# Kernel tuning notes

Measured on AMD Instinct MI355X. Metric: run time of the kernel, lower is better.

Reference implementation:

```python
import jax, jax.numpy as jnp
import numpy as np

B, C_IN, H, W_SP = 16, 128, 56, 56
C_OUT, KH, KW = 256, 3, 3
STRIDE = (1, 1)
PADDING = (1, 1)


def setup_inputs() -> dict:
    key = jax.random.key(0)
    kx, kw = jax.random.split(key)
    x = jax.random.normal(kx, (B, C_IN, H, W_SP), dtype=jnp.float32)
    W = jax.random.normal(kw, (C_OUT, C_IN, KH, KW), dtype=jnp.float32) * 0.01
    b = jnp.zeros((C_OUT,), dtype=jnp.float32)
    return {"x": x, "W": W, "b": b}


def reference(x, W, b):
    # NCHW direct convolution, same math as the nested-loop torch module.
    out = jax.lax.conv_general_dilated(
        x, W,
        window_strides=STRIDE,
        padding=[(PADDING[0], PADDING[0]), (PADDING[1], PADDING[1])],
        dimension_numbers=("NCHW", "OIHW", "NCHW"),
    )
    return out + b[None, :, None, None]
```

## Files before the change

kernel.cpp:

```cpp
#include <hip/hip_runtime.h>

typedef __attribute__((ext_vector_type(8))) short short8;
typedef __attribute__((ext_vector_type(4))) float f32x4;

#define CI    128
#define CO_   256
#define HW_   56
#define PLANE 3136
#define NB    16
#define STOT  50176
#define KTOT  1152
#define OUTN  802816

#define XT_BYTES   12845056ull
#define WP_USHORTS 294912
#define WS_NEED    (12845056ull + 589824ull + 256ull)

__device__ __forceinline__ unsigned short f2bf(float f) {
  unsigned u = __float_as_uint(f);
  u += 0x7FFFu + ((u >> 16) & 1u);
  return (unsigned short)(u >> 16);
}

__device__ __forceinline__ void gload16(void* lds, const void* g) {
  __builtin_amdgcn_global_load_lds(
      (const __attribute__((address_space(1))) unsigned int*)g,
      (__attribute__((address_space(3))) unsigned int*)lds, 16, 0, 0);
}

template <int N> __device__ __forceinline__ void vmwait() {
  asm volatile("s_waitcnt vmcnt(%0)" ::"n"(N) : "memory");
}

__global__ __launch_bounds__(256) void prep_fused(const float* __restrict__ X,
                                                  const float* __restrict__ W,
                                                  unsigned short* __restrict__ Xt,
                                                  unsigned short* __restrict__ Wp) {
  const int t = threadIdx.x;
  if (blockIdx.x < 1600) {
    __shared__ __align__(16) unsigned short tile[32][132];
    const int bx = blockIdx.x;
    const int n   = bx / 100;
    const int rem = bx % 100;
    const int cib = rem / 25;
    const int spb = rem % 25;
    const int sp0 = spb * 128;
    const float* src = X + (size_t)(n * CI + cib * 32) * PLANE;
#pragma unroll
    for (int j = 0; j < 4; ++j) {
      int f = t + 256 * j;
      int ci  = f >> 5;
      int sp4 = (f & 31) * 4;
      if (sp0 + sp4 < PLANE) {
        f32x4 v = *(const f32x4*)(src + (size_t)ci * PLANE + sp0 + sp4);
#pragma unroll
        for (int e = 0; e < 4; ++e) tile[ci][sp4 + e] = f2bf(v[e]);
      }
    }
    __syncthreads();
    unsigned short* dst = Xt + ((size_t)n * PLANE + sp0) * CI + cib * 32;
#pragma unroll
    for (int j = 0; j < 2; ++j) {
      int g = t + 256 * j;
      int sp = g >> 2;
      int q  = g & 3;
      if (sp0 + sp < PLANE) {
        short8 v;
#pragma unroll
        for (int e = 0; e < 8; ++e) v[e] = (short)tile[q * 8 + e][sp];
        *(short8*)(dst + (size_t)sp * CI + q * 8) = v;
      }
    }
  } else {
    const int u = (blockIdx.x - 1600) * 256 + t;
    const int rcbmt = u >> 9;
    const int p     = u & 511;
    const int mt  = rcbmt & 1;
    const int rcb = rcbmt >> 1;
    const int cb  = rcb & 3;
    const int r   = rcb >> 2;
    const int col = p >> 2;
    const int kg  = (p & 3) ^ ((col >> 1) & 3);
    const int co  = mt * 128 + col;
    const int ci0 = cb * 32 + kg * 8;
    short8 v;
#pragma unroll
    for (int e = 0; e < 8; ++e)
      v[e] = (short)f2bf(W[(size_t)co * KTOT + (size_t)(ci0 + e) * 9 + r]);
    *(short8*)(Wp + (size_t)u * 8) = v;
    if (u < 16) {
      short8 z = {0, 0, 0, 0, 0, 0, 0, 0};
      *(short8*)(Wp + WP_USHORTS + u * 8) = z;
    }
  }
}

__global__ __launch_bounds__(512, 2) void conv_gemm(const unsigned short* __restrict__ Xt,
                                                    const unsigned short* __restrict__ Wp,
                                                    const float* __restrict__ bias,
                                                    float* __restrict__ out) {
  __shared__ __align__(1024) char smem[131072];
  const int t    = threadIdx.x;
  const int lane = t & 63;
  const int wid  = t >> 6;
  const int wm   = wid >> 2, wn = wid & 3;

  const int orig = blockIdx.x;
  const int xcd = orig & 7, idx = orig >> 3;
  const int spt = (xcd < 4 ? xcd * 25 : 100 + (xcd - 4) * 24) + idx;

  const int kgB = (t & 3) ^ ((t >> 3) & 3);
  const int S0 = spt * 256 + (t >> 2);
  const int S1 = S0 + 128;
  const int hw0 = S0 % PLANE, h0 = hw0 / HW_, w0 = hw0 - h0 * HW_;
  const int hw1 = S1 % PLANE, h1 = hw1 / HW_, w1 = hw1 - h1 * HW_;
  int vm0 = 0, vm1 = 0;
#pragma unroll
  for (int r = 0; r < 9; ++r) {
    int dh = r / 3 - 1, dw = r % 3 - 1;
    vm0 |= (int)(((unsigned)(h0 + dh) < HW_) & ((unsigned)(w0 + dw) < HW_)) << r;
    vm1 |= (int)(((unsigned)(h1 + dh) < HW_) & ((unsigned)(w1 + dw) < HW_)) << r;
  }
  const char* xb0 = (const char*)Xt + ((size_t)S0 * CI + kgB * 8) * 2;
  const char* xb1 = (const char*)Xt + ((size_t)S1 * CI + kgB * 8) * 2;
  const char* zb  = (const char*)(Wp + WP_USHORTS) + (t & 3) * 16;
  const char* wpA = (const char*)Wp + t * 16;

  const int swz  = ((lane >> 4) ^ ((lane >> 1) & 3)) * 16;
  const int aoff = (wm * 128 + (lane & 15)) * 64 + swz;
  const int boff = 16384 + (wn * 64 + (lane & 15)) * 64 + swz;

  f32x4 acc[8][4];
  const f32x4 zf = {0.f, 0.f, 0.f, 0.f};
#pragma unroll
  for (int m = 0; m < 8; ++m)
#pragma unroll
    for (int n = 0; n < 4; ++n) acc[m][n] = zf;

  auto SA = [&](int s1, int j, char* buf) {
    gload16(buf + j * 8192 + wid * 1024, wpA + (size_t)s1 * 16384 + j * 8192);
  };
  auto SB = [&](int s1, int j, char* buf) {
    const int r = s1 >> 2, cb = s1 & 3;
    const int dh = r / 3 - 1, dw = r % 3 - 1;
    const int ro = dh * HW_ + dw;
    const bool v = ((j ? vm1 : vm0) >> r) & 1;
    const char* src = (j ? xb1 : xb0) + ro * 256 + cb * 64;
    gload16(buf + 16384 + j * 8192 + wid * 1024, v ? src : zb);
  };
  auto STAGE = [&](int s1) {
    char* nb = smem + (s1 & 3) * 32768;
    SA(s1, 0, nb); SA(s1, 1, nb); SB(s1, 0, nb); SB(s1, 1, nb);
  };

  STAGE(0); STAGE(1); STAGE(2);

#pragma unroll
  for (int s = 0; s < 36; ++s) {
    if (s <= 34) vmwait<4>();
    else         vmwait<0>();
    __builtin_amdgcn_s_barrier();

    if (s <= 32) STAGE(s + 3);

    const char* rb = smem + (s & 3) * 32768;
    short8 bF[4];
#pragma unroll
    for (int n = 0; n < 4; ++n) bF[n] = *(const short8*)(rb + boff + n * 1024);

    __builtin_amdgcn_s_setprio(1);
#pragma unroll
    for (int m = 0; m < 8; ++m) {
      short8 aFm = *(const short8*)(rb + aoff + m * 1024);
#pragma unroll
      for (int n = 0; n < 4; ++n)
        acc[m][n] = __builtin_amdgcn_mfma_f32_16x16x32_bf16(aFm, bF[n], acc[m][n], 0, 0, 0);
    }
    __builtin_amdgcn_s_setprio(0);
  }

#pragma unroll
  for (int nf = 0; nf < 4; ++nf) {
    int S = spt * 256 + wn * 64 + nf * 16 + (lane & 15);
    int nimg = S / PLANE, hw = S - nimg * PLANE;
    float* ob = out + (size_t)nimg * OUTN + hw;
#pragma unroll
    for (int mf = 0; mf < 8; ++mf) {
      int cob = wm * 128 + mf * 16 + (lane >> 4) * 4;
#pragma unroll
      for (int r2 = 0; r2 < 4; ++r2)
        ob[(size_t)(cob + r2) * PLANE] = acc[mf][nf][r2] + bias[cob + r2];
    }
  }
}

__global__ __launch_bounds__(256) void conv_naive(const float* __restrict__ X,
                                                  const float* __restrict__ W,
                                                  const float* __restrict__ bias,
                                                  float* __restrict__ out) {
  int idx = blockIdx.x * 256 + threadIdx.x;
  int hw = idx % PLANE;
  int co = (idx / PLANE) & 255;
  int n  = idx / (PLANE * 256);
  int h = hw / HW_, w = hw - h * HW_;
  float acc = bias[co];
  const float* xp = X + (size_t)n * CI * PLANE;
  const float* wp = W + (size_t)co * KTOT;
  for (int ci = 0; ci < CI; ++ci) {
#pragma unroll
    for (int kh = 0; kh < 3; ++kh) {
      int y = h + kh - 1;
      if ((unsigned)y >= HW_) continue;
#pragma unroll
      for (int kw = 0; kw < 3; ++kw) {
        int x = w + kw - 1;
        if ((unsigned)x >= HW_) continue;
        acc += xp[(size_t)ci * PLANE + y * HW_ + x] * wp[ci * 9 + kh * 3 + kw];
      }
    }
  }
  out[idx] = acc;
}

extern "C" void kernel_launch(void* const* d_in, const int* in_sizes, int n_in,
                              void* d_out, int out_size, void* d_ws, size_t ws_size,
                              hipStream_t stream) {
  (void)in_sizes; (void)n_in; (void)out_size;
  const float* X = (const float*)d_in[0];
  const float* W = (const float*)d_in[1];
  const float* b = (const float*)d_in[2];
  float* out = (float*)d_out;
  if (ws_size >= WS_NEED) {
    unsigned short* Xt = (unsigned short*)d_ws;
    unsigned short* Wp = (unsigned short*)((char*)d_ws + XT_BYTES);
    prep_fused<<<1744, 256, 0, stream>>>(X, W, Xt, Wp);
    conv_gemm<<<196, 512, 0, stream>>>(Xt, Wp, b, out);
  } else {
    conv_naive<<<(NB * CO_ * PLANE + 255) / 256, 256, 0, stream>>>(X, W, b, out);
  }
}
```

Measured before the change: 50.76 us.

## Restructure conv GEMM main loop into two-stage k-tiles with phased MFMA quadrants

```diff
diff --git a/kernel.cpp b/kernel.cpp
--- a/kernel.cpp
+++ b/kernel.cpp
@@ -30,6 +30,9 @@
 
 template <int N> __device__ __forceinline__ void vmwait() {
   asm volatile("s_waitcnt vmcnt(%0)" ::"n"(N) : "memory");
+}
+__device__ __forceinline__ void lgkm0() {
+  asm volatile("s_waitcnt lgkmcnt(0)" ::: "memory");
 }
 
 __global__ __launch_bounds__(256) void prep_fused(const float* __restrict__ X,
@@ -95,6 +98,15 @@
   }
 }
 
+#define MFMA16(MBASE, NBASE)                                                            \
+  __builtin_amdgcn_s_setprio(1);                                                        \
+  _Pragma("unroll") for (int k = 0; k < 2; ++k)                                         \
+  _Pragma("unroll") for (int m = 0; m < 4; ++m)                                         \
+  _Pragma("unroll") for (int n = 0; n < 2; ++n)                                         \
+    acc[(MBASE) + m][(NBASE) + n] = __builtin_amdgcn_mfma_f32_16x16x32_bf16(            \
+        aF[m][k], bF[(NBASE) + n][k], acc[(MBASE) + m][(NBASE) + n], 0, 0, 0);          \
+  __builtin_amdgcn_s_setprio(0);
+
 __global__ __launch_bounds__(512, 2) void conv_gemm(const unsigned short* __restrict__ Xt,
                                                     const unsigned short* __restrict__ Wp,
                                                     const float* __restrict__ bias,
@@ -137,10 +149,12 @@
 #pragma unroll
     for (int n = 0; n < 4; ++n) acc[m][n] = zf;
 
-  auto SA = [&](int s1, int j, char* buf) {
+  auto SA = [&](int s1, int j) {
+    char* buf = smem + (s1 & 3) * 32768;
     gload16(buf + j * 8192 + wid * 1024, wpA + (size_t)s1 * 16384 + j * 8192);
   };
-  auto SB = [&](int s1, int j, char* buf) {
+  auto SB = [&](int s1, int j) {
+    char* buf = smem + (s1 & 3) * 32768;
     const int r = s1 >> 2, cb = s1 & 3;
     const int dh = r / 3 - 1, dw = r % 3 - 1;
     const int ro = dh * HW_ + dw;
@@ -148,35 +162,61 @@
     const char* src = (j ? xb1 : xb0) + ro * 256 + cb * 64;
     gload16(buf + 16384 + j * 8192 + wid * 1024, v ? src : zb);
   };
-  auto STAGE = [&](int s1) {
-    char* nb = smem + (s1 & 3) * 32768;
-    SA(s1, 0, nb); SA(s1, 1, nb); SB(s1, 0, nb); SB(s1, 1, nb);
-  };
-
-  STAGE(0); STAGE(1); STAGE(2);
-
-#pragma unroll
-  for (int s = 0; s < 36; ++s) {
-    if (s <= 34) vmwait<4>();
-    else         vmwait<0>();
-    __builtin_amdgcn_s_barrier();
-
-    if (s <= 32) STAGE(s + 3);
-
-    const char* rb = smem + (s & 3) * 32768;
-    short8 bF[4];
-#pragma unroll
-    for (int n = 0; n < 4; ++n) bF[n] = *(const short8*)(rb + boff + n * 1024);
-
-    __builtin_amdgcn_s_setprio(1);
-#pragma unroll
-    for (int m = 0; m < 8; ++m) {
-      short8 aFm = *(const short8*)(rb + aoff + m * 1024);
-#pragma unroll
-      for (int n = 0; n < 4; ++n)
-        acc[m][n] = __builtin_amdgcn_mfma_f32_16x16x32_bf16(aFm, bF[n], acc[m][n], 0, 0, 0);
-    }
-    __builtin_amdgcn_s_setprio(0);
+  auto STAGE = [&](int s1) { SA(s1, 0); SA(s1, 1); SB(s1, 0); SB(s1, 1); };
+
+  STAGE(0); STAGE(1); STAGE(2); STAGE(3);
+
+#pragma unroll
+  for (int kt = 0; kt < 18; ++kt) {
+    const char* rb0 = smem + ((2 * kt) & 3) * 32768;
+    const char* rb1 = smem + ((2 * kt + 1) & 3) * 32768;
+    const char* ca0 = rb0 + aoff;
+    const char* ca1 = rb1 + aoff;
+    const char* cb0 = rb0 + boff;
+    const char* cb1 = rb1 + boff;
+    short8 aF[4][2], bF[4][2];
+
+    if (kt <= 16) vmwait<8>();
+    else          vmwait<0>();
+    __builtin_amdgcn_s_barrier();
+#pragma unroll
+    for (int m = 0; m < 4; ++m) {
+      aF[m][0] = *(const short8*)(ca0 + m * 1024);
+      aF[m][1] = *(const short8*)(ca1 + m * 1024);
+    }
+#pragma unroll
+    for (int n = 0; n < 2; ++n) {
+      bF[n][0] = *(const short8*)(cb0 + n * 1024);
+      bF[n][1] = *(const short8*)(cb1 + n * 1024);
+    }
+    lgkm0();
+    MFMA16(0, 0)
+    __builtin_amdgcn_s_barrier();
+
+#pragma unroll
+    for (int n = 0; n < 2; ++n) {
+      bF[2 + n][0] = *(const short8*)(cb0 + (2 + n) * 1024);
+      bF[2 + n][1] = *(const short8*)(cb1 + (2 + n) * 1024);
+    }
+    __builtin_amdgcn_s_barrier();
+    lgkm0();
+    MFMA16(0, 2)
+    __builtin_amdgcn_s_barrier();
+
+#pragma unroll
+    for (int m = 0; m < 4; ++m) {
+      aF[m][0] = *(const short8*)(ca0 + (4 + m) * 1024);
+      aF[m][1] = *(const short8*)(ca1 + (4 + m) * 1024);
+    }
+    __builtin_amdgcn_s_barrier();
+    lgkm0();
+    MFMA16(4, 2)
+    __builtin_amdgcn_s_barrier();
+
+    if (kt <= 15) { STAGE(2 * kt + 4); STAGE(2 * kt + 5); }
+    __builtin_amdgcn_s_barrier();
+    MFMA16(4, 0)
+    __builtin_amdgcn_s_barrier();
   }
 
 #pragma unroll
```

Measured after the change: 55.77 us. 1.1x slower.
